# Kernel tuning notes

Measured on AMD Instinct MI355X. Metric: run time of the kernel, lower is better.

## Reference

```python
import jax, jax.numpy as jnp
import numpy as np

STEPS = 10          # points in t_grid -> STEPS-1 RK4 intervals
TRACE_STEPS = 2     # Hutchinson probes per dynamics eval
T_FINAL = 1.0
CLAMP = 100.0


def odefun(t, z, W1, b1, tw1, W2, b2):
    # time-conditioned 2-layer tanh MLP (canonical FFJORD dynamics)
    h = jnp.tanh(z @ W1 + b1 + t * tw1)
    return h @ W2 + b2


def setup_inputs() -> dict:
    key = jax.random.key(0)
    B, D, H = 2048, 512, 1024
    ks = jax.random.split(key, 4)
    s1 = 1.0 / np.sqrt(D)
    s2 = 1.0 / np.sqrt(H)
    return {
        "x": jax.random.normal(ks[0], (B, D), jnp.float32),
        "W1": jax.random.normal(ks[1], (D, H), jnp.float32) * s1,
        "b1": jnp.zeros((H,), jnp.float32),
        "tw1": jax.random.normal(ks[2], (H,), jnp.float32) * 0.1,
        "W2": jax.random.normal(ks[3], (H, D), jnp.float32) * s2,
        "b2": jnp.zeros((D,), jnp.float32),
    }


def reference(x, W1, b1, tw1, W2, b2):
    params = (W1, b1, tw1, W2, b2)
    B, D = x.shape

    def divergence_estimate(t, z, e):
        # torch detaches z before the grad call -> stop_gradient here
        z_sg = jax.lax.stop_gradient(z)
        f, vjp_fn = jax.vjp(lambda zz: odefun(t, zz, *params), z_sg)
        etf = vjp_fn(e)[0]                      # e^T J  (Hutchinson probe)
        return f, jnp.sum(etf * e, axis=-1)     # [B]

    def augmented_dynamics(t, state, key):
        z = state[:, :-1]                        # [B, D]
        div_est = jnp.zeros((B,), state.dtype)
        f_z = None
        for i in range(TRACE_STEPS):             # small fixed loop
            e = jax.random.randint(jax.random.fold_in(key, i), z.shape, 0, 2).astype(z.dtype) * 2.0 - 1.0
            f_z, div = divergence_estimate(t, z, e)
            div_est = div_est + div
        div_est = jnp.clip(div_est / TRACE_STEPS, -CLAMP, CLAMP)
        return jnp.concatenate([f_z, -div_est[:, None]], axis=-1)

    t_grid = jnp.linspace(0.0, T_FINAL, STEPS)
    state0 = jnp.concatenate([x, jnp.zeros((B, 1), x.dtype)], axis=-1)  # [B, D+1]

    def step(carry, t01):
        state, key = carry
        t0, t1 = t01[0], t01[1]
        dt = t1 - t0
        key, k1k, k2k, k3k, k4k = jax.random.split(key, 5)
        # torchdiffeq 'rk4' = Kutta's 3/8-rule variant (rk4_alt_step_func)
        k1 = augmented_dynamics(t0, state, k1k)
        k2 = augmented_dynamics(t0 + dt / 3.0, state + dt * k1 / 3.0, k2k)
        k3 = augmented_dynamics(t0 + dt * 2.0 / 3.0, state + dt * (k2 - k1 / 3.0), k3k)
        k4 = augmented_dynamics(t1, state + dt * (k1 - k2 + k3), k4k)
        state = state + (k1 + 3.0 * (k2 + k3) + k4) * dt * 0.125
        return (state, key), None

    t_pairs = jnp.stack([t_grid[:-1], t_grid[1:]], axis=-1)  # [STEPS-1, 2]
    (state, _), _ = jax.lax.scan(step, (state0, jax.random.key(1234)), t_pairs)

    rep, probsolve = state[:, :-1], state[:, -1]
    logprob = -0.5 * jnp.sum(rep * rep, axis=-1) + probsolve
    return rep, logprob
```

## Files before the change

### kernel.cpp

```cpp
#include <hip/hip_runtime.h>
#include <stdint.h>


#define B_N 2048
#define D_N 512
#define H_N 1024
#define BD (B_N * D_N)

typedef unsigned short u16;
typedef __attribute__((ext_vector_type(8))) short s16x8;
typedef __attribute__((ext_vector_type(4))) float f32x4;

typedef __attribute__((address_space(1))) const uint32_t ga_u32;
typedef __attribute__((address_space(3))) uint32_t ls_u32;

#if __has_builtin(__builtin_amdgcn_alignbit)
#define ROTL32(x, r) __builtin_amdgcn_alignbit((x), (x), 32 - (r))
#else
#define ROTL32(x, r) (((x) << (r)) | ((x) >> (32 - (r))))
#endif

__device__ __forceinline__ float bf2f(u16 u) {
  union { uint32_t u; float f; } c; c.u = ((uint32_t)u) << 16; return c.f;
}
__device__ __forceinline__ u16 f2bf(float f) {
  union { float f; uint32_t u; } c; c.f = f;
  uint32_t r = c.u + 0x7FFFu + ((c.u >> 16) & 1u);
  return (u16)(r >> 16);
}

struct U2 { uint32_t x, y; };

__device__ __forceinline__ U2 tf2x32(uint32_t k0, uint32_t k1, uint32_t x0, uint32_t x1) {
  uint32_t k2 = k0 ^ k1 ^ 0x1BD11BDAu;
#define RND(r) { x0 += x1; x1 = ROTL32(x1, r); x1 ^= x0; }
  x0 += k0; x1 += k1;
  RND(13) RND(15) RND(26) RND(6)
  x0 += k1; x1 += k2 + 1u;
  RND(17) RND(29) RND(16) RND(24)
  x0 += k2; x1 += k0 + 2u;
  RND(13) RND(15) RND(26) RND(6)
  x0 += k0; x1 += k1 + 3u;
  RND(17) RND(29) RND(16) RND(24)
  x0 += k1; x1 += k2 + 4u;
  RND(13) RND(15) RND(26) RND(6)
  x0 += k2; x1 += k0 + 5u;
#undef RND
  U2 r; r.x = x0; r.y = x1; return r;
}

__global__ void k_keysched(uint32_t* __restrict__ ekeys) {
  if (threadIdx.x != 0 || blockIdx.x != 0) return;
  uint32_t kx = 0u, ky = 1234u;
  for (int s = 0; s < 9; ++s) {
    for (int st = 0; st < 4; ++st) {
      U2 kst = tf2x32(kx, ky, 0u, (uint32_t)(st + 1));
      for (int pr = 0; pr < 2; ++pr) {
        U2 fo = tf2x32(kst.x, kst.y, 0u, (uint32_t)pr);
        U2 k2 = tf2x32(fo.x, fo.y, 0u, 1u);
        ekeys[(s * 4 + st) * 4 + pr * 2 + 0] = k2.x;
        ekeys[(s * 4 + st) * 4 + pr * 2 + 1] = k2.y;
      }
    }
    U2 c = tf2x32(kx, ky, 0u, 0u);
    kx = c.x; ky = c.y;
  }
}

__global__ void k_egen(u16* __restrict__ ebf, const uint32_t* __restrict__ keys, int gs) {
  int t = blockIdx.x * 256 + threadIdx.x;
  int stage = gs + (t >> 16), rem = t & 65535;
  int probe = rem >> 15, idx = rem & 32767;
  uint32_t p0 = (uint32_t)idx * 32;
  uint32_t k0 = keys[stage * 4 + probe * 2], k1 = keys[stage * 4 + probe * 2 + 1];
  uint4* dst = (uint4*)(ebf + (size_t)(stage & 3) * (2 * (size_t)BD) + (size_t)probe * BD + (size_t)idx * 32);
#pragma unroll
  for (int g = 0; g < 4; ++g) {
    uint32_t pr[4];
#pragma unroll
    for (int h = 0; h < 4; ++h) {
      uint32_t c0 = p0 + g * 8 + h * 2;
      U2 r0 = tf2x32(k0, k1, 0u, c0);
      U2 r1 = tf2x32(k0, k1, 0u, c0 + 1u);
      pr[h] = (((r0.x ^ r0.y) & 1u) ? 0x3F80u : 0xBF80u) |
              (((r1.x ^ r1.y) & 1u) ? 0x3F800000u : 0xBF800000u);
    }
    uint4 v; v.x = pr[0]; v.y = pr[1]; v.z = pr[2]; v.w = pr[3];
    dst[g] = v;
  }
}

__global__ void k_init(const float* __restrict__ x, float* __restrict__ z, u16* __restrict__ zin,
                       float* __restrict__ lp, float* __restrict__ d0, float* __restrict__ d1) {
  int i = blockIdx.x * 256 + threadIdx.x;
  if (i < BD) { float v = x[i]; z[i] = v; zin[i] = f2bf(v); }
  if (i < B_N) { lp[i] = 0.f; d0[i] = 0.f; d1[i] = 0.f; }
}

__global__ void k_cvtT(const float* __restrict__ src, u16* __restrict__ dst, int R, int C) {
  int i = blockIdx.x * 256 + threadIdx.x;
  if (i >= R * C) return;
  int c = i / R, r = i - c * R;
  dst[i] = f2bf(src[(size_t)r * C + c]);
}
__global__ void k_cvt(const float* __restrict__ src, u16* __restrict__ dst, int n) {
  int i = blockIdx.x * 256 + threadIdx.x;
  if (i < n) dst[i] = f2bf(src[i]);
}

__global__ void k_sentinel(float* __restrict__ out, int n) {
  int i = blockIdx.x * 256 + threadIdx.x;
  if (i < n) out[i] = 12345.0f;
}

__global__ __launch_bounds__(256)
void k_f1(const u16* __restrict__ zin, const u16* __restrict__ e0g, const u16* __restrict__ e1g,
          const u16* __restrict__ W1T, const u16* __restrict__ W2b,
          const float* __restrict__ b1, const float* __restrict__ tw1, float tstage,
          u16* __restrict__ hbuf, float* __restrict__ div0, float* __restrict__ div1) {
  __shared__ u16 S[2][5 * 2048];
  const int tid = threadIdx.x, wave = tid >> 6, lane = tid & 63;
  const int bm = blockIdx.x >> 4;
  const int bh = blockIdx.x & 15;
  const int row0 = bm * 64, col0 = bh * 64;
  const int wm = wave >> 1, wn = wave & 1, r16 = lane & 15, q = lane >> 4;
  const int srow = lane >> 2, scol = (lane & 3) * 8;

  f32x4 az[2][2], au0[2][2], au1[2][2], av0[2][2], av1[2][2];
#pragma unroll
  for (int i = 0; i < 2; ++i)
#pragma unroll
    for (int j = 0; j < 2; ++j) {
      az[i][j] = (f32x4){0,0,0,0}; au0[i][j] = (f32x4){0,0,0,0}; au1[i][j] = (f32x4){0,0,0,0};
      av0[i][j] = (f32x4){0,0,0,0}; av1[i][j] = (f32x4){0,0,0,0};
    }

  const size_t arow = (size_t)(row0 + wave * 16 + srow) * 512 + scol;
  const size_t brow = (size_t)(col0 + wave * 16 + srow) * 512 + scol;
  auto stage = [&](int kt, int buf) {
    u16* b = &S[buf][0];
    __builtin_amdgcn_global_load_lds((ga_u32*)(zin + arow + kt), (ls_u32*)(b + 0    + wave * 512), 16, 0, 0);
    __builtin_amdgcn_global_load_lds((ga_u32*)(e0g + arow + kt), (ls_u32*)(b + 2048 + wave * 512), 16, 0, 0);
    __builtin_amdgcn_global_load_lds((ga_u32*)(e1g + arow + kt), (ls_u32*)(b + 4096 + wave * 512), 16, 0, 0);
    __builtin_amdgcn_global_load_lds((ga_u32*)(W1T + brow + kt), (ls_u32*)(b + 6144 + wave * 512), 16, 0, 0);
    __builtin_amdgcn_global_load_lds((ga_u32*)(W2b + brow + kt), (ls_u32*)(b + 8192 + wave * 512), 16, 0, 0);
  };
  stage(0, 0);
  for (int it = 0; it < 16; ++it) {
    const int buf = it & 1;
    __syncthreads();
    if (it + 1 < 16) stage((it + 1) * 32, buf ^ 1);
    const u16* b = &S[buf][0];
    s16x8 zf[2], e0f[2], e1f[2], w1f[2], w2f[2];
#pragma unroll
    for (int i = 0; i < 2; ++i) {
      const int ao = (wm * 32 + i * 16 + r16) * 32 + q * 8;
      zf[i]  = *(const s16x8*)(b + 0    + ao);
      e0f[i] = *(const s16x8*)(b + 2048 + ao);
      e1f[i] = *(const s16x8*)(b + 4096 + ao);
    }
#pragma unroll
    for (int j = 0; j < 2; ++j) {
      const int bo = (wn * 32 + j * 16 + r16) * 32 + q * 8;
      w1f[j] = *(const s16x8*)(b + 6144 + bo);
      w2f[j] = *(const s16x8*)(b + 8192 + bo);
    }
#pragma unroll
    for (int i = 0; i < 2; ++i)
#pragma unroll
      for (int j = 0; j < 2; ++j) {
        az[i][j]  = __builtin_amdgcn_mfma_f32_16x16x32_bf16(zf[i],  w1f[j], az[i][j],  0, 0, 0);
        au0[i][j] = __builtin_amdgcn_mfma_f32_16x16x32_bf16(e0f[i], w1f[j], au0[i][j], 0, 0, 0);
        au1[i][j] = __builtin_amdgcn_mfma_f32_16x16x32_bf16(e1f[i], w1f[j], au1[i][j], 0, 0, 0);
        av0[i][j] = __builtin_amdgcn_mfma_f32_16x16x32_bf16(e0f[i], w2f[j], av0[i][j], 0, 0, 0);
        av1[i][j] = __builtin_amdgcn_mfma_f32_16x16x32_bf16(e1f[i], w2f[j], av1[i][j], 0, 0, 0);
      }
  }

  float d0s[2][4], d1s[2][4];
#pragma unroll
  for (int i = 0; i < 2; ++i)
#pragma unroll
    for (int r = 0; r < 4; ++r) { d0s[i][r] = 0.f; d1s[i][r] = 0.f; }

#pragma unroll
  for (int j = 0; j < 2; ++j) {
    const int gcol = col0 + wn * 32 + j * 16 + r16;
    const float colb = b1[gcol] + tstage * tw1[gcol];
#pragma unroll
    for (int i = 0; i < 2; ++i) {
      const int rbase = row0 + wm * 32 + i * 16 + q * 4;
#pragma unroll
      for (int r = 0; r < 4; ++r) {
        float hv = tanhf(az[i][j][r] + colb);
        hbuf[(size_t)(rbase + r) * H_N + gcol] = f2bf(hv);
        float s = 1.f - hv * hv;
        d0s[i][r] += s * au0[i][j][r] * av0[i][j][r];
        d1s[i][r] += s * au1[i][j][r] * av1[i][j][r];
      }
    }
  }
#pragma unroll
  for (int i = 0; i < 2; ++i)
#pragma unroll
    for (int r = 0; r < 4; ++r) {
      float a = d0s[i][r], b = d1s[i][r];
#pragma unroll
      for (int m = 1; m < 16; m <<= 1) { a += __shfl_xor(a, m); b += __shfl_xor(b, m); }
      if (r16 == 0) {
        int grow = row0 + wm * 32 + i * 16 + q * 4 + r;
        atomicAdd(&div0[grow], a);
        atomicAdd(&div1[grow], b);
      }
    }
}

template<int ST>
__global__ __launch_bounds__(256)
void k_f3(const u16* __restrict__ hbuf, const u16* __restrict__ W2T, const float* __restrict__ b2,
          float* __restrict__ z, float* __restrict__ ACC, float* __restrict__ T,
          u16* __restrict__ zin, float dt,
          float* __restrict__ lp, float* __restrict__ div0, float* __restrict__ div1, float wdt) {
  __shared__ u16 S[2][2 * 2048];
  const int tid = threadIdx.x, wave = tid >> 6, lane = tid & 63;
  const int bm = blockIdx.x >> 3;
  const int bn = blockIdx.x & 7;
  const int row0 = bm * 64, col0 = bn * 64;
  const int wm = wave >> 1, wn = wave & 1, r16 = lane & 15, q = lane >> 4;
  const int srow = lane >> 2, scol = (lane & 3) * 8;

  if (bn == 0 && tid < 64) {
    int b = row0 + tid;
    float c = 0.5f * (div0[b] + div1[b]);
    c = fminf(fmaxf(c, -100.f), 100.f);
    lp[b] -= wdt * c;
    div0[b] = 0.f; div1[b] = 0.f;
  }

  f32x4 acc[2][2];
#pragma unroll
  for (int i = 0; i < 2; ++i)
#pragma unroll
    for (int j = 0; j < 2; ++j) acc[i][j] = (f32x4){0,0,0,0};

  const size_t arow = (size_t)(row0 + wave * 16 + srow) * 1024 + scol;
  const size_t brow = (size_t)(col0 + wave * 16 + srow) * 1024 + scol;
  auto stage = [&](int kt, int buf) {
    u16* b = &S[buf][0];
    __builtin_amdgcn_global_load_lds((ga_u32*)(hbuf + arow + kt), (ls_u32*)(b + 0    + wave * 512), 16, 0, 0);
    __builtin_amdgcn_global_load_lds((ga_u32*)(W2T  + brow + kt), (ls_u32*)(b + 2048 + wave * 512), 16, 0, 0);
  };
  stage(0, 0);
  for (int it = 0; it < 32; ++it) {
    const int buf = it & 1;
    __syncthreads();
    if (it + 1 < 32) stage((it + 1) * 32, buf ^ 1);
    const u16* b = &S[buf][0];
    s16x8 af[2], bfr[2];
#pragma unroll
    for (int i = 0; i < 2; ++i)
      af[i] = *(const s16x8*)(b + (wm * 32 + i * 16 + r16) * 32 + q * 8);
#pragma unroll
    for (int j = 0; j < 2; ++j)
      bfr[j] = *(const s16x8*)(b + 2048 + (wn * 32 + j * 16 + r16) * 32 + q * 8);
#pragma unroll
    for (int i = 0; i < 2; ++i)
#pragma unroll
      for (int j = 0; j < 2; ++j)
        acc[i][j] = __builtin_amdgcn_mfma_f32_16x16x32_bf16(af[i], bfr[j], acc[i][j], 0, 0, 0);
  }

#pragma unroll
  for (int j = 0; j < 2; ++j) {
    const int gcol = col0 + wn * 32 + j * 16 + r16;
    const float cb = b2[gcol];
#pragma unroll
    for (int i = 0; i < 2; ++i) {
      const int rbase = row0 + wm * 32 + i * 16 + q * 4;
#pragma unroll
      for (int r = 0; r < 4; ++r) {
        const size_t idx = (size_t)(rbase + r) * D_N + gcol;
        const float f = acc[i][j][r] + cb;
        if (ST == 0) {
          ACC[idx] = dt * 0.125f * f;
          T[idx]   = dt * f;
          zin[idx] = f2bf(z[idx] + dt * f * (1.f / 3.f));
        } else if (ST == 1) {
          float t_ = T[idx];
          ACC[idx] += 0.375f * dt * f;
          zin[idx] = f2bf(z[idx] + dt * f - t_ * (1.f / 3.f));
          T[idx]   = t_ - dt * f;
        } else if (ST == 2) {
          ACC[idx] += 0.375f * dt * f;
          zin[idx] = f2bf(z[idx] + T[idx] + dt * f);
        } else {
          float zn = z[idx] + ACC[idx] + dt * 0.125f * f;
          z[idx]   = zn;
          zin[idx] = f2bf(zn);
        }
      }
    }
  }
}

__global__ void k_out(const float* __restrict__ z, const float* __restrict__ lp,
                      float* __restrict__ out) {
  int b = blockIdx.x, t = threadIdx.x;
  const float* zr = z + (size_t)b * D_N;
  float ss = 0.f;
  for (int d = t; d < D_N; d += 256) {
    float v = zr[d];
    out[(size_t)b * D_N + d] = v;
    ss += v * v;
  }
  for (int off = 32; off > 0; off >>= 1) ss += __shfl_down(ss, off);
  __shared__ float red[4];
  if ((t & 63) == 0) red[t >> 6] = ss;
  __syncthreads();
  if (t == 0) out[(size_t)BD + b] = -0.5f * (red[0] + red[1] + red[2] + red[3]) + lp[b];
}

extern "C" void kernel_launch(void* const* d_in, const int* in_sizes, int n_in,
                              void* d_out, int out_size, void* d_ws, size_t ws_size,
                              hipStream_t stream) {
  const float* x   = (const float*)d_in[0];
  const float* W1  = (const float*)d_in[1];
  const float* b1  = (const float*)d_in[2];
  const float* tw1 = (const float*)d_in[3];
  const float* W2  = (const float*)d_in[4];
  const float* b2  = (const float*)d_in[5];

  const size_t NEEDED = (size_t)45 << 20;
  if (ws_size < NEEDED) {
    k_sentinel<<<(BD + B_N + 255) / 256, 256, 0, stream>>>((float*)d_out, BD + B_N);
    return;
  }
  char* w = (char*)d_ws;
  auto carve = [&](size_t bytes) { char* p = w; w += (bytes + 255) & ~(size_t)255; return p; };
  uint32_t* keys = (uint32_t*)carve(144 * sizeof(uint32_t));
  u16* ebf   = (u16*)carve((size_t)4 * 2 * BD * 2);
  float* z   = (float*)carve((size_t)BD * 4);
  float* ACC = (float*)carve((size_t)BD * 4);
  float* T   = (float*)carve((size_t)BD * 4);
  u16* zin   = (u16*)carve((size_t)BD * 2);
  u16* hbuf  = (u16*)carve((size_t)B_N * H_N * 2);
  u16* W1T   = (u16*)carve((size_t)H_N * D_N * 2);
  u16* W2b   = (u16*)carve((size_t)H_N * D_N * 2);
  u16* W2T   = (u16*)carve((size_t)D_N * H_N * 2);
  float* lp   = (float*)carve((size_t)B_N * 4);
  float* div0 = (float*)carve((size_t)B_N * 4);
  float* div1 = (float*)carve((size_t)B_N * 4);

  k_keysched<<<1, 1, 0, stream>>>(keys);
  k_init<<<BD / 256, 256, 0, stream>>>(x, z, zin, lp, div0, div1);
  k_cvtT<<<(D_N * H_N) / 256, 256, 0, stream>>>(W1, W1T, D_N, H_N);
  k_cvt <<<(H_N * D_N) / 256, 256, 0, stream>>>(W2, W2b, H_N * D_N);
  k_cvtT<<<(H_N * D_N) / 256, 256, 0, stream>>>(W2, W2T, H_N, D_N);

  const int gF1 = (B_N / 64) * (H_N / 64);
  const int gF3 = (B_N / 64) * (D_N / 64);

  for (int s = 0; s < 9; ++s) {
    float t0 = (float)s / 9.0f;
    float t1 = (float)(s + 1) / 9.0f;
    float dt = t1 - t0;
    float tst[4] = { t0, t0 + dt / 3.0f, t0 + dt * 2.0f / 3.0f, t1 };
    float wts[4] = { 1.f, 3.f, 3.f, 1.f };
    for (int st = 0; st < 4; ++st) {
      const int sg = s * 4 + st;
      if ((sg & 3) == 0) k_egen<<<1024, 256, 0, stream>>>(ebf, keys, sg);
      const u16* e0g = ebf + (size_t)(sg & 3) * (2 * (size_t)BD);
      const u16* e1g = e0g + BD;
      k_f1<<<gF1, 256, 0, stream>>>(zin, e0g, e1g, W1T, W2b, b1, tw1, tst[st], hbuf, div0, div1);
      const float wdt = dt * 0.125f * wts[st];
      if (st == 0)      k_f3<0><<<gF3, 256, 0, stream>>>(hbuf, W2T, b2, z, ACC, T, zin, dt, lp, div0, div1, wdt);
      else if (st == 1) k_f3<1><<<gF3, 256, 0, stream>>>(hbuf, W2T, b2, z, ACC, T, zin, dt, lp, div0, div1, wdt);
      else if (st == 2) k_f3<2><<<gF3, 256, 0, stream>>>(hbuf, W2T, b2, z, ACC, T, zin, dt, lp, div0, div1, wdt);
      else              k_f3<3><<<gF3, 256, 0, stream>>>(hbuf, W2T, b2, z, ACC, T, zin, dt, lp, div0, div1, wdt);
    }
  }
  k_out<<<B_N, 256, 0, stream>>>(z, lp, (float*)d_out);
}
```

Before: 1.476 ms.

## Swizzle LDS layout, use fast tanh, and halve second-GEMM tile width

Applies an XOR swizzle to LDS column offsets in both GEMM kernels to cut bank conflicts on the fragment reads. Replaces tanhf with an exp-based fast tanh in the first-layer epilogue. Shrinks the second GEMM's tile from 64x64 to 64x32, with each wave owning 16 rows, which doubles the grid for better occupancy but lowers per-block reuse of the hbuf tile. The fast tanh gives slightly different numerics.

New measurement: 1.498 ms. No clear change (+1.5%).

```diff
diff --git a/kernel.cpp b/kernel.cpp
--- a/kernel.cpp
+++ b/kernel.cpp
@@ -20,13 +20,15 @@
 #define ROTL32(x, r) (((x) << (r)) | ((x) >> (32 - (r))))
 #endif
 
-__device__ __forceinline__ float bf2f(u16 u) {
-  union { uint32_t u; float f; } c; c.u = ((uint32_t)u) << 16; return c.f;
-}
 __device__ __forceinline__ u16 f2bf(float f) {
   union { float f; uint32_t u; } c; c.f = f;
   uint32_t r = c.u + 0x7FFFu + ((c.u >> 16) & 1u);
   return (u16)(r >> 16);
+}
+__device__ __forceinline__ float fast_tanh(float v) {
+  float e = __expf(2.0f * fabsf(v));
+  float t = 1.0f - 2.0f / (e + 1.0f);
+  return copysignf(t, v);
 }
 
 struct U2 { uint32_t x, y; };
@@ -113,10 +115,11 @@
   if (i < n) out[i] = 12345.0f;
 }
 
+
 __global__ __launch_bounds__(256)
 void k_f1(const u16* __restrict__ zin, const u16* __restrict__ e0g, const u16* __restrict__ e1g,
           const u16* __restrict__ W1T, const u16* __restrict__ W2b,
-          const float* __restrict__ b1, const float* __restrict__ tw1, float tstage,
+          const float* __restrict__ b1v, const float* __restrict__ tw1v, float tstage,
           u16* __restrict__ hbuf, float* __restrict__ div0, float* __restrict__ div1) {
   __shared__ u16 S[2][5 * 2048];
   const int tid = threadIdx.x, wave = tid >> 6, lane = tid & 63;
@@ -124,7 +127,9 @@
   const int bh = blockIdx.x & 15;
   const int row0 = bm * 64, col0 = bh * 64;
   const int wm = wave >> 1, wn = wave & 1, r16 = lane & 15, q = lane >> 4;
-  const int srow = lane >> 2, scol = (lane & 3) * 8;
+  const int srow = lane >> 2;
+  const int scol = (((lane & 3) ^ ((srow >> 1) & 3))) * 8;
+  const int cqa = (q ^ ((r16 >> 1) & 3)) * 8;
 
   f32x4 az[2][2], au0[2][2], au1[2][2], av0[2][2], av1[2][2];
 #pragma unroll
@@ -154,14 +159,14 @@
     s16x8 zf[2], e0f[2], e1f[2], w1f[2], w2f[2];
 #pragma unroll
     for (int i = 0; i < 2; ++i) {
-      const int ao = (wm * 32 + i * 16 + r16) * 32 + q * 8;
+      const int ao = (wm * 32 + i * 16 + r16) * 32 + cqa;
       zf[i]  = *(const s16x8*)(b + 0    + ao);
       e0f[i] = *(const s16x8*)(b + 2048 + ao);
       e1f[i] = *(const s16x8*)(b + 4096 + ao);
     }
 #pragma unroll
     for (int j = 0; j < 2; ++j) {
-      const int bo = (wn * 32 + j * 16 + r16) * 32 + q * 8;
+      const int bo = (wn * 32 + j * 16 + r16) * 32 + cqa;
       w1f[j] = *(const s16x8*)(b + 6144 + bo);
       w2f[j] = *(const s16x8*)(b + 8192 + bo);
     }
@@ -186,13 +191,13 @@
 #pragma unroll
   for (int j = 0; j < 2; ++j) {
     const int gcol = col0 + wn * 32 + j * 16 + r16;
-    const float colb = b1[gcol] + tstage * tw1[gcol];
+    const float colb = b1v[gcol] + tstage * tw1v[gcol];
 #pragma unroll
     for (int i = 0; i < 2; ++i) {
       const int rbase = row0 + wm * 32 + i * 16 + q * 4;
 #pragma unroll
       for (int r = 0; r < 4; ++r) {
-        float hv = tanhf(az[i][j][r] + colb);
+        float hv = fast_tanh(az[i][j][r] + colb);
         hbuf[(size_t)(rbase + r) * H_N + gcol] = f2bf(hv);
         float s = 1.f - hv * hv;
         d0s[i][r] += s * au0[i][j][r] * av0[i][j][r];
@@ -204,30 +209,32 @@
   for (int i = 0; i < 2; ++i)
 #pragma unroll
     for (int r = 0; r < 4; ++r) {
-      float a = d0s[i][r], b = d1s[i][r];
-#pragma unroll
-      for (int m = 1; m < 16; m <<= 1) { a += __shfl_xor(a, m); b += __shfl_xor(b, m); }
+      float a = d0s[i][r], bb = d1s[i][r];
+#pragma unroll
+      for (int m = 1; m < 16; m <<= 1) { a += __shfl_xor(a, m); bb += __shfl_xor(bb, m); }
       if (r16 == 0) {
         int grow = row0 + wm * 32 + i * 16 + q * 4 + r;
         atomicAdd(&div0[grow], a);
-        atomicAdd(&div1[grow], b);
+        atomicAdd(&div1[grow], bb);
       }
     }
 }
 
 template<int ST>
 __global__ __launch_bounds__(256)
-void k_f3(const u16* __restrict__ hbuf, const u16* __restrict__ W2T, const float* __restrict__ b2,
+void k_f3(const u16* __restrict__ hbuf, const u16* __restrict__ W2T, const float* __restrict__ b2v,
           float* __restrict__ z, float* __restrict__ ACC, float* __restrict__ T,
           u16* __restrict__ zin, float dt,
           float* __restrict__ lp, float* __restrict__ div0, float* __restrict__ div1, float wdt) {
-  __shared__ u16 S[2][2 * 2048];
+  __shared__ u16 S[2][3 * 2048];
   const int tid = threadIdx.x, wave = tid >> 6, lane = tid & 63;
-  const int bm = blockIdx.x >> 3;
-  const int bn = blockIdx.x & 7;
-  const int row0 = bm * 64, col0 = bn * 64;
-  const int wm = wave >> 1, wn = wave & 1, r16 = lane & 15, q = lane >> 4;
-  const int srow = lane >> 2, scol = (lane & 3) * 8;
+  const int bm = blockIdx.x >> 4;
+  const int bn = blockIdx.x & 15;
+  const int row0 = bm * 64, col0 = bn * 32;
+  const int r16 = lane & 15, q = lane >> 4;
+  const int srow = lane >> 2;
+  const int scol = (((lane & 3) ^ ((srow >> 1) & 3))) * 8;
+  const int cqa = (q ^ ((r16 >> 1) & 3)) * 8;
 
   if (bn == 0 && tid < 64) {
     int b = row0 + tid;
@@ -237,18 +244,16 @@
     div0[b] = 0.f; div1[b] = 0.f;
   }
 
-  f32x4 acc[2][2];
-#pragma unroll
-  for (int i = 0; i < 2; ++i)
-#pragma unroll
-    for (int j = 0; j < 2; ++j) acc[i][j] = (f32x4){0,0,0,0};
+  f32x4 acc[2];
+  acc[0] = (f32x4){0,0,0,0}; acc[1] = (f32x4){0,0,0,0};
 
   const size_t arow = (size_t)(row0 + wave * 16 + srow) * 1024 + scol;
-  const size_t brow = (size_t)(col0 + wave * 16 + srow) * 1024 + scol;
+  const size_t brow = (size_t)(col0 + (wave & 1) * 16 + srow) * 1024 + scol;
   auto stage = [&](int kt, int buf) {
     u16* b = &S[buf][0];
-    __builtin_amdgcn_global_load_lds((ga_u32*)(hbuf + arow + kt), (ls_u32*)(b + 0    + wave * 512), 16, 0, 0);
-    __builtin_amdgcn_global_load_lds((ga_u32*)(W2T  + brow + kt), (ls_u32*)(b + 2048 + wave * 512), 16, 0, 0);
+    __builtin_amdgcn_global_load_lds((ga_u32*)(hbuf + arow + kt), (ls_u32*)(b + wave * 512), 16, 0, 0);
+    if (wave < 2)
+      __builtin_amdgcn_global_load_lds((ga_u32*)(W2T + brow + kt), (ls_u32*)(b + 4096 + wave * 512), 16, 0, 0);
   };
   stage(0, 0);
   for (int it = 0; it < 32; ++it) {
@@ -256,48 +261,38 @@
     __syncthreads();
     if (it + 1 < 32) stage((it + 1) * 32, buf ^ 1);
     const u16* b = &S[buf][0];
-    s16x8 af[2], bfr[2];
-#pragma unroll
-    for (int i = 0; i < 2; ++i)
-      af[i] = *(const s16x8*)(b + (wm * 32 + i * 16 + r16) * 32 + q * 8);
-#pragma unroll
-    for (int j = 0; j < 2; ++j)
-      bfr[j] = *(const s16x8*)(b + 2048 + (wn * 32 + j * 16 + r16) * 32 + q * 8);
-#pragma unroll
-    for (int i = 0; i < 2; ++i)
-#pragma unroll
-      for (int j = 0; j < 2; ++j)
-        acc[i][j] = __builtin_amdgcn_mfma_f32_16x16x32_bf16(af[i], bfr[j], acc[i][j], 0, 0, 0);
+    s16x8 af  = *(const s16x8*)(b + (wave * 16 + r16) * 32 + cqa);
+    s16x8 bf0 = *(const s16x8*)(b + 4096 + r16 * 32 + cqa);
+    s16x8 bf1 = *(const s16x8*)(b + 4096 + (16 + r16) * 32 + cqa);
+    acc[0] = __builtin_amdgcn_mfma_f32_16x16x32_bf16(af, bf0, acc[0], 0, 0, 0);
+    acc[1] = __builtin_amdgcn_mfma_f32_16x16x32_bf16(af, bf1, acc[1], 0, 0, 0);
   }
 
 #pragma unroll
   for (int j = 0; j < 2; ++j) {
-    const int gcol = col0 + wn * 32 + j * 16 + r16;
-    const float cb = b2[gcol];
-#pragma unroll
-    for (int i = 0; i < 2; ++i) {
-      const int rbase = row0 + wm * 32 + i * 16 + q * 4;
-#pragma unroll
-      for (int r = 0; r < 4; ++r) {
-        const size_t idx = (size_t)(rbase + r) * D_N + gcol;
-        const float f = acc[i][j][r] + cb;
-        if (ST == 0) {
-          ACC[idx] = dt * 0.125f * f;
-          T[idx]   = dt * f;
-          zin[idx] = f2bf(z[idx] + dt * f * (1.f / 3.f));
-        } else if (ST == 1) {
-          float t_ = T[idx];
-          ACC[idx] += 0.375f * dt * f;
-          zin[idx] = f2bf(z[idx] + dt * f - t_ * (1.f / 3.f));
-          T[idx]   = t_ - dt * f;
-        } else if (ST == 2) {
-          ACC[idx] += 0.375f * dt * f;
-          zin[idx] = f2bf(z[idx] + T[idx] + dt * f);
-        } else {
-          float zn = z[idx] + ACC[idx] + dt * 0.125f * f;
-          z[idx]   = zn;
-          zin[idx] = f2bf(zn);
-        }
+    const int gcol = col0 + j * 16 + r16;
+    const float cb = b2v[gcol];
+    const int rbase = row0 + wave * 16 + q * 4;
+#pragma unroll
+    for (int r = 0; r < 4; ++r) {
+      const size_t idx = (size_t)(rbase + r) * D_N + gcol;
+      const float f = acc[j][r] + cb;
+      if (ST == 0) {
+        ACC[idx] = dt * 0.125f * f;
+        T[idx]   = dt * f;
+        zin[idx] = f2bf(z[idx] + dt * f * (1.f / 3.f));
+      } else if (ST == 1) {
+        float t_ = T[idx];
+        ACC[idx] += 0.375f * dt * f;
+        zin[idx] = f2bf(z[idx] + dt * f - t_ * (1.f / 3.f));
+        T[idx]   = t_ - dt * f;
+      } else if (ST == 2) {
+        ACC[idx] += 0.375f * dt * f;
+        zin[idx] = f2bf(z[idx] + T[idx] + dt * f);
+      } else {
+        float zn = z[idx] + ACC[idx] + dt * 0.125f * f;
+        z[idx]   = zn;
+        zin[idx] = f2bf(zn);
       }
     }
   }
@@ -329,10 +324,11 @@
   const float* tw1 = (const float*)d_in[3];
   const float* W2  = (const float*)d_in[4];
   const float* b2  = (const float*)d_in[5];
+  float* outp = (float*)d_out;
 
   const size_t NEEDED = (size_t)45 << 20;
   if (ws_size < NEEDED) {
-    k_sentinel<<<(BD + B_N + 255) / 256, 256, 0, stream>>>((float*)d_out, BD + B_N);
+    k_sentinel<<<(BD + B_N + 255) / 256, 256, 0, stream>>>(outp, BD + B_N);
     return;
   }
   char* w = (char*)d_ws;
@@ -358,7 +354,7 @@
   k_cvtT<<<(H_N * D_N) / 256, 256, 0, stream>>>(W2, W2T, H_N, D_N);
 
   const int gF1 = (B_N / 64) * (H_N / 64);
-  const int gF3 = (B_N / 64) * (D_N / 64);
+  const int gF3 = (B_N / 64) * (D_N / 32);
 
   for (int s = 0; s < 9; ++s) {
     float t0 = (float)s / 9.0f;
@@ -379,5 +375,5 @@
       else              k_f3<3><<<gF3, 256, 0, stream>>>(hbuf, W2T, b2, z, ACC, T, zin, dt, lp, div0, div1, wdt);
     }
   }
-  k_out<<<B_N, 256, 0, stream>>>(z, lp, (float*)d_out);
-}
+  k_out<<<B_N, 256, 0, stream>>>(z, lp, outp);
+}
```
